# Kernel optimization log

Measured on AMD Instinct MI355X. Metric: run time of the kernel, lower is better.

Reference implementation:

```python
import jax, jax.numpy as jnp
import numpy as np

B, S, D, H = 2, 2048, 768, 12
DK = D // H
NEG = -1e9

def setup_inputs() -> dict:
    key = jax.random.key(0)
    ks = jax.random.split(key, 12)
    def lin(k):
        kw, kb = jax.random.split(k)
        lim = 1.0 / np.sqrt(D)
        W = jax.random.uniform(kw, (D, D), jnp.float32, -lim, lim)
        b = jax.random.uniform(kb, (D,), jnp.float32, -lim, lim)
        return W, b
    Wq, bq = lin(ks[0]); Wk, bk = lin(ks[1]); Wv, bv = lin(ks[2]); Wo, bo = lin(ks[3])
    query = jax.random.normal(ks[4], (B, S, D), jnp.float32)
    key_t = jax.random.normal(ks[5], (B, S, D), jnp.float32)
    value = jax.random.normal(ks[6], (B, S, D), jnp.float32)
    mask = jax.random.randint(ks[7], (B, S, S), 0, 2, jnp.int32)
    return {"query": query, "key": key_t, "value": value, "mask": mask,
            "Wq": Wq, "bq": bq, "Wk": Wk, "bk": bk, "Wv": Wv, "bv": bv,
            "Wo": Wo, "bo": bo}

def reference(query, key, value, mask, Wq, bq, Wk, bk, Wv, bv, Wo, bo):
    # project and split heads: [B,S,D] -> [B,H,S,DK]
    def proj(x, W, b):
        return (x @ W.T + b).reshape(B, S, H, DK).transpose(0, 2, 1, 3)
    q = proj(query, Wq, bq)
    k = proj(key, Wk, bk)
    v = proj(value, Wv, bv)
    scale = np.float32(1.0 / np.sqrt(DK))
    scores = jnp.einsum('bhqd,bhkd->bhqk', q, k) * scale  # [B,H,S,S]
    scores = jnp.where(mask[:, None, :, :] == 0, jnp.float32(NEG), scores)
    log_attn = jax.nn.log_softmax(scores, axis=-1)  # [B,H,S,S]
    p_attn = jnp.exp(log_attn)                      # softmax, shares reduction
    x = jnp.einsum('bhqk,bhkd->bhqd', p_attn, v)    # [B,H,S,DK]
    x = x.transpose(0, 2, 1, 3).reshape(B, S, D)
    out = x @ Wo.T + bo
    return out, log_attn
```

## Files before the change

kernel.cpp:

```cpp
#include <hip/hip_runtime.h>

#define B_ 2
#define S_ 2048
#define D_ 768
#define H_ 12
#define DK_ 64
#define BH_ (B_*H_)
#define NEGV (-1e9f)
#define SCALE 0.125f
#define MINIT (-1e30f)

typedef unsigned short u16;
typedef unsigned long long u64;
typedef __attribute__((ext_vector_type(8))) short bf16x8;
typedef __attribute__((ext_vector_type(4))) float f32x4;
typedef __attribute__((ext_vector_type(4))) int   i32x4;

__device__ __forceinline__ u16 f2bf(float f){
  union { float f; unsigned int i; } v; v.f = f;
  unsigned int x = v.i;
  return (u16)((x + 0x7FFFu + ((x >> 16) & 1u)) >> 16);
}
__device__ __forceinline__ void split2(float x, u16& h, u16& l){
  const unsigned int xi = __float_as_uint(x);
  h = (u16)(xi >> 16);
  const float lo = x - __uint_as_float(xi & 0xFFFF0000u);
  l = (u16)(__float_as_uint(lo) >> 16);
}

#define XN_ ((size_t)4096*768)
#define WN_ ((size_t)768*768)

__global__ __launch_bounds__(256) void prep(
    const float* __restrict__ Xq, const float* __restrict__ Xk, const float* __restrict__ Xv,
    const float* __restrict__ Wq, const float* __restrict__ Wk, const float* __restrict__ Wv,
    const int* __restrict__ mask,
    u16* __restrict__ scr, u64* __restrict__ mbits)
{
  const int a = blockIdx.y;
  if (a == 6){
    const size_t nw = (size_t)B_*S_*(S_/64);
    for (size_t wi = (size_t)blockIdx.x*256 + threadIdx.x; wi < nw; wi += (size_t)gridDim.x*256){
      const int* mp = mask + wi*64;
      u64 v = 0;
      #pragma unroll
      for (int j=0;j<64;j+=4){
        i32x4 m4 = __builtin_nontemporal_load((const i32x4*)(mp + j));
        v |= ((u64)(m4.x!=0) << j)     | ((u64)(m4.y!=0) << (j+1))
           | ((u64)(m4.z!=0) << (j+2)) | ((u64)(m4.w!=0) << (j+3));
      }
      mbits[wi] = v;
    }
    return;
  }
  const float* src; u16* h; u16* l; size_t n;
  if (a < 3){
    src = (a==0)?Xq:(a==1)?Xk:Xv;
    h = scr + (size_t)a*XN_;  l = scr + (size_t)(3+a)*XN_;  n = XN_;
  } else {
    const int z = a-3;
    src = (z==0)?Wq:(z==1)?Wk:Wv;
    h = scr + 6*XN_ + (size_t)z*WN_;  l = scr + 6*XN_ + 3*WN_ + (size_t)z*WN_;  n = WN_;
  }
  const size_t nv = n >> 2;
  for (size_t i = (size_t)blockIdx.x*256 + threadIdx.x; i < nv; i += (size_t)gridDim.x*256){
    f32x4 v = __builtin_nontemporal_load((const f32x4*)src + i);
    ushort4 hv, lv;
    split2(v.x,hv.x,lv.x); split2(v.y,hv.y,lv.y); split2(v.z,hv.z,lv.z); split2(v.w,hv.w,lv.w);
    ((ushort4*)h)[i] = hv;  ((ushort4*)l)[i] = lv;
  }
}

template<bool ALO, bool BPRE, int OMODE>
__device__ __forceinline__ void gemmM(const u16* __restrict__ Ah_, const u16* __restrict__ Al_,
                                      const u16* __restrict__ Bh_, const u16* __restrict__ Bl_,
                                      const float* __restrict__ Bf_,
                                      const float* __restrict__ bias, void* __restrict__ outp)
{
  const int bx = blockIdx.x, by = blockIdx.y;
  const int tid  = threadIdx.x;
  const int lane = tid & 63;
  const int w    = tid >> 6;
  const int g    = lane >> 4;
  const int c    = lane & 15;
  const int wr   = w >> 1, wc = w & 1;

  __shared__ u16 Ah[128][36];
  __shared__ u16 Al[128][36];
  __shared__ u16 Bh[128][36];
  __shared__ u16 Bl[128][36];

  const int ar0 = (OMODE==2 ? by : bx) * 128;
  const int br0 = (OMODE==2 ? bx : by) * 128;

  const int prow = tid >> 2;
  const int pcol = (tid & 3) * 8;
  const int frow = tid >> 3;
  const int fcol = (tid & 7) * 4;

  uint4 rAh0, rAh1, rAl0, rAl1, rBh0, rBh1, rBl0, rBl1;
  float4 rf0, rf1, rf2, rf3;

  f32x4 acc[4][4];
  #pragma unroll
  for (int m=0;m<4;m++)
    #pragma unroll
    for (int n=0;n<4;n++) acc[m][n] = (f32x4){0.f,0.f,0.f,0.f};

#define LD_TILE(k0) do{ \
    rAh0 = *(const uint4*)(Ah_ + (size_t)(ar0+prow)*D_ + (k0) + pcol); \
    rAh1 = *(const uint4*)(Ah_ + (size_t)(ar0+64+prow)*D_ + (k0) + pcol); \
    if constexpr (ALO){ \
      rAl0 = *(const uint4*)(Al_ + (size_t)(ar0+prow)*D_ + (k0) + pcol); \
      rAl1 = *(const uint4*)(Al_ + (size_t)(ar0+64+prow)*D_ + (k0) + pcol); } \
    if constexpr (BPRE){ \
      rBh0 = *(const uint4*)(Bh_ + (size_t)(br0+prow)*D_ + (k0) + pcol); \
      rBh1 = *(const uint4*)(Bh_ + (size_t)(br0+64+prow)*D_ + (k0) + pcol); \
      rBl0 = *(const uint4*)(Bl_ + (size_t)(br0+prow)*D_ + (k0) + pcol); \
      rBl1 = *(const uint4*)(Bl_ + (size_t)(br0+64+prow)*D_ + (k0) + pcol); \
    } else { \
      rf0 = *(const float4*)(Bf_ + (size_t)(br0+frow)*D_ + (k0) + fcol); \
      rf1 = *(const float4*)(Bf_ + (size_t)(br0+32+frow)*D_ + (k0) + fcol); \
      rf2 = *(const float4*)(Bf_ + (size_t)(br0+64+frow)*D_ + (k0) + fcol); \
      rf3 = *(const float4*)(Bf_ + (size_t)(br0+96+frow)*D_ + (k0) + fcol); \
    } }while(0)

#define ST_F32(rf, rofs) do{ \
    ushort4 hv, lv; \
    split2((rf).x,hv.x,lv.x); split2((rf).y,hv.y,lv.y); \
    split2((rf).z,hv.z,lv.z); split2((rf).w,hv.w,lv.w); \
    *(ushort4*)&Bh[(rofs)+frow][fcol] = hv;  *(ushort4*)&Bl[(rofs)+frow][fcol] = lv; }while(0)

#define ST_TILE() do{ \
    *(uint4*)&Ah[prow][pcol] = rAh0;  *(uint4*)&Ah[prow+64][pcol] = rAh1; \
    if constexpr (ALO){ *(uint4*)&Al[prow][pcol] = rAl0; *(uint4*)&Al[prow+64][pcol] = rAl1; } \
    if constexpr (BPRE){ \
      *(uint4*)&Bh[prow][pcol] = rBh0;  *(uint4*)&Bh[prow+64][pcol] = rBh1; \
      *(uint4*)&Bl[prow][pcol] = rBl0;  *(uint4*)&Bl[prow+64][pcol] = rBl1; \
    } else { ST_F32(rf0,0); ST_F32(rf1,32); ST_F32(rf2,64); ST_F32(rf3,96); } }while(0)

  LD_TILE(0);

  for (int t=0; t<D_/32; ++t){
    __syncthreads();
    ST_TILE();
    if (t < D_/32 - 1) LD_TILE((t+1)*32);
    __syncthreads();

    bf16x8 fah[4], fal[4], fbh[4], fbl[4];
    #pragma unroll
    for (int m=0;m<4;m++){
      fah[m] = *(const bf16x8*)&Ah[wr*64 + m*16 + c][g*8];
      if constexpr (ALO) fal[m] = *(const bf16x8*)&Al[wr*64 + m*16 + c][g*8];
    }
    #pragma unroll
    for (int n=0;n<4;n++){
      fbh[n] = *(const bf16x8*)&Bh[wc*64 + n*16 + c][g*8];
      fbl[n] = *(const bf16x8*)&Bl[wc*64 + n*16 + c][g*8];
    }
    #pragma unroll
    for (int m=0;m<4;m++)
      #pragma unroll
      for (int n=0;n<4;n++){
        acc[m][n] = __builtin_amdgcn_mfma_f32_16x16x32_bf16(fah[m], fbh[n], acc[m][n], 0,0,0);
        acc[m][n] = __builtin_amdgcn_mfma_f32_16x16x32_bf16(fah[m], fbl[n], acc[m][n], 0,0,0);
        if constexpr (ALO)
          acc[m][n] = __builtin_amdgcn_mfma_f32_16x16x32_bf16(fal[m], fbh[n], acc[m][n], 0,0,0);
      }
  }
#undef LD_TILE
#undef ST_F32
#undef ST_TILE

  if constexpr (OMODE==0) {
    float* out = (float*)outp;
    float bb[4];
    #pragma unroll
    for (int n=0;n<4;n++) bb[n] = bias[br0 + wc*64 + n*16 + c];
    #pragma unroll
    for (int m=0;m<4;m++)
      #pragma unroll
      for (int r=0;r<4;r++){
        const int rg = ar0 + wr*64 + m*16 + g*4 + r;
        #pragma unroll
        for (int n=0;n<4;n++)
          out[(size_t)rg*D_ + br0 + wc*64 + n*16 + c] = acc[m][n][r] + bb[n];
      }
  } else if constexpr (OMODE==1) {
    u16* out = (u16*)outp;
    float bb[4];
    #pragma unroll
    for (int n=0;n<4;n++) bb[n] = bias[br0 + wc*64 + n*16 + c];
    #pragma unroll
    for (int m=0;m<4;m++)
      #pragma unroll
      for (int r=0;r<4;r++){
        const int rg = ar0 + wr*64 + m*16 + g*4 + r;
        const int batch = rg >> 11, s = rg & (S_-1);
        #pragma unroll
        for (int n=0;n<4;n++){
          const int col = br0 + wc*64 + n*16 + c;
          const int hh = col >> 6, dk = col & 63;
          out[((size_t)(batch*H_ + hh)*S_ + s)*DK_ + dk] = f2bf(acc[m][n][r] + bb[n]);
        }
      }
  } else {
    u16* out = (u16*)outp;
    #pragma unroll
    for (int m=0;m<4;m++)
      #pragma unroll
      for (int r=0;r<4;r++){
        const int dkg = ar0 + wr*64 + m*16 + g*4 + r;
        const int hh = dkg >> 6, dkl = dkg & 63;
        const float bb = bias[dkg];
        #pragma unroll
        for (int n=0;n<4;n++){
          const int sg = br0 + wc*64 + n*16 + c;
          const int batch = sg >> 11, s = sg & (S_-1);
          out[((size_t)(batch*H_ + hh)*DK_ + dkl)*S_ + s] = f2bf(acc[m][n][r] + bb);
        }
      }
  }
}

__global__ __launch_bounds__(256,2) void proj_qkv(
    const u16* __restrict__ scr,
    const float* __restrict__ bq, const float* __restrict__ bk, const float* __restrict__ bv,
    u16* __restrict__ qkv)
{
  const int z = blockIdx.z;
  u16* out = qkv + (size_t)z * ((size_t)BH_*S_*DK_);
  const u16* Xh = scr + (size_t)z*XN_;
  const u16* Xl = scr + (size_t)(3+z)*XN_;
  const u16* Wh = scr + 6*XN_ + (size_t)z*WN_;
  const u16* Wl = scr + 6*XN_ + 3*WN_ + (size_t)z*WN_;
  const float* bias = (z==0)?bq:(z==1)?bk:bv;
  if (z==2) gemmM<true,true,2>(Wh, Wl, Xh, Xl, nullptr, bias, (void*)out);
  else      gemmM<true,true,1>(Xh, Xl, Wh, Wl, nullptr, bias, (void*)out);
}

__global__ __launch_bounds__(256,2) void proj_o(
    const u16* __restrict__ Xc, const float* __restrict__ Wo, const float* __restrict__ bo,
    float* __restrict__ out)
{
  gemmM<false,false,0>(Xc, nullptr, nullptr, nullptr, Wo, bo, (void*)out);
}

__global__ __launch_bounds__(256,3) void attn(const u16* __restrict__ qkv,
                                              const u64* __restrict__ mbits,
                                              float* __restrict__ la, u16* __restrict__ ctx)
{
  const int bh = blockIdx.y;
  const int q0 = blockIdx.x * 64;
  const int b = bh / H_;
  const int h = bh - b*H_;
  const u16* Qp = qkv + (size_t)bh * S_ * DK_;
  const u16* Kp = qkv + (size_t)(BH_ + bh) * S_ * DK_;
  const u16* Vt = qkv + (size_t)(2*BH_ + bh) * S_ * DK_;
  const u64* Mb = mbits + (size_t)b * S_ * (S_/64);

  const int tid  = threadIdx.x;
  const int w    = tid >> 6;
  const int lane = tid & 63;
  const int g    = lane >> 4;
  const int c    = lane & 15;
  const int srow = tid >> 3;
  const int scol = (tid & 7) * 8;

  __shared__ u16 KsB[2][64][72];
  __shared__ u16 VsB[2][64][72];
  __shared__ u16 Ps[4][16][72];

  {
    uint4 qa = *(const uint4*)(Qp + (size_t)(q0+srow)*DK_ + scol);
    uint4 qb = *(const uint4*)(Qp + (size_t)(q0+32+srow)*DK_ + scol);
    *(uint4*)&VsB[0][srow][scol] = qa;
    *(uint4*)&VsB[0][srow+32][scol] = qb;
  }
  __syncthreads();
  const bf16x8 qf0 = *(const bf16x8*)&VsB[0][w*16 + c][g*8];
  const bf16x8 qf1 = *(const bf16x8*)&VsB[0][w*16 + c][g*8 + 32];

  float mt[4], lt[4];
  #pragma unroll
  for (int r=0;r<4;r++){ mt[r] = MINIT; lt[r] = 0.f; }

  {
    uint4 ka = *(const uint4*)(Kp + (size_t)srow*DK_ + scol);
    uint4 kb = *(const uint4*)(Kp + (size_t)(32+srow)*DK_ + scol);
    *(uint4*)&KsB[0][srow][scol] = ka;
    *(uint4*)&KsB[0][srow+32][scol] = kb;
    for (int t=0; t<S_/64; ++t){
      __syncthreads();
      if (t < S_/64-1){
        const u16* kp = Kp + (size_t)(t+1)*64*DK_;
        ka = *(const uint4*)(kp + (size_t)srow*DK_ + scol);
        kb = *(const uint4*)(kp + (size_t)(32+srow)*DK_ + scol);
      }
      u64 mw[4];
      #pragma unroll
      for (int r=0;r<4;r++) mw[r] = Mb[(size_t)(q0 + w*16 + g*4 + r)*(S_/64) + t];

      f32x4 sc[4];
      __builtin_amdgcn_s_setprio(1);
      #pragma unroll
      for (int nt=0; nt<4; nt++){
        const bf16x8 kf0 = *(const bf16x8*)&KsB[t&1][nt*16 + c][g*8];
        const bf16x8 kf1 = *(const bf16x8*)&KsB[t&1][nt*16 + c][g*8 + 32];
        f32x4 z = {0.f,0.f,0.f,0.f};
        z      = __builtin_amdgcn_mfma_f32_16x16x32_bf16(qf0, kf0, z, 0,0,0);
        sc[nt] = __builtin_amdgcn_mfma_f32_16x16x32_bf16(qf1, kf1, z, 0,0,0);
      }
      __builtin_amdgcn_s_setprio(0);
      #pragma unroll
      for (int r=0;r<4;r++){
        const float sv0 = ((mw[r] >> (c    )) & 1) ? sc[0][r]*SCALE : NEGV;
        const float sv1 = ((mw[r] >> (c+16)) & 1) ? sc[1][r]*SCALE : NEGV;
        const float sv2 = ((mw[r] >> (c+32)) & 1) ? sc[2][r]*SCALE : NEGV;
        const float sv3 = ((mw[r] >> (c+48)) & 1) ? sc[3][r]*SCALE : NEGV;
        const float cm = fmaxf(fmaxf(sv0,sv1), fmaxf(sv2,sv3));
        if (!__all(cm <= mt[r])){
          const float mn = fmaxf(mt[r], cm);
          lt[r] *= __expf(mt[r]-mn);
          mt[r] = mn;
        }
        lt[r] += __expf(sv0-mt[r]) + __expf(sv1-mt[r]) + __expf(sv2-mt[r]) + __expf(sv3-mt[r]);
      }
      if (t < S_/64-1){
        *(uint4*)&KsB[(t+1)&1][srow][scol] = ka;
        *(uint4*)&KsB[(t+1)&1][srow+32][scol] = kb;
      }
    }
  }

  float ml[4];
  #pragma unroll
  for (int r=0;r<4;r++){
    float m = mt[r], l = lt[r];
    #pragma unroll
    for (int st=1; st<16; st<<=1){
      const float m2 = __shfl_xor(m, st);
      const float l2 = __shfl_xor(l, st);
      const float mn = fmaxf(m, m2);
      l = l*__expf(m-mn) + l2*__expf(m2-mn);
      m = mn;
    }
    ml[r] = m + __logf(fmaxf(l, 1e-30f));
  }

  f32x4 o[4];
  #pragma unroll
  for (int nt=0;nt<4;nt++) o[nt] = (f32x4){0.f,0.f,0.f,0.f};

  {
    uint4 ka = *(const uint4*)(Kp + (size_t)srow*DK_ + scol);
    uint4 kb = *(const uint4*)(Kp + (size_t)(32+srow)*DK_ + scol);
    uint4 va = *(const uint4*)(Vt + (size_t)srow*S_ + scol);
    uint4 vb = *(const uint4*)(Vt + (size_t)(32+srow)*S_ + scol);
    *(uint4*)&KsB[0][srow][scol] = ka;   *(uint4*)&KsB[0][srow+32][scol] = kb;
    *(uint4*)&VsB[0][srow][scol] = va;   *(uint4*)&VsB[0][srow+32][scol] = vb;
    for (int t=0; t<S_/64; ++t){
      __syncthreads();
      if (t < S_/64-1){
        const u16* kp = Kp + (size_t)(t+1)*64*DK_;
        const u16* vp = Vt + (size_t)(t+1)*64;
        ka = *(const uint4*)(kp + (size_t)srow*DK_ + scol);
        kb = *(const uint4*)(kp + (size_t)(32+srow)*DK_ + scol);
        va = *(const uint4*)(vp + (size_t)srow*S_ + scol);
        vb = *(const uint4*)(vp + (size_t)(32+srow)*S_ + scol);
      }
      u64 mw[4];
      #pragma unroll
      for (int r=0;r<4;r++) mw[r] = Mb[(size_t)(q0 + w*16 + g*4 + r)*(S_/64) + t];

      f32x4 sc[4];
      __builtin_amdgcn_s_setprio(1);
      #pragma unroll
      for (int nt=0; nt<4; nt++){
        const bf16x8 kf0 = *(const bf16x8*)&KsB[t&1][nt*16 + c][g*8];
        const bf16x8 kf1 = *(const bf16x8*)&KsB[t&1][nt*16 + c][g*8 + 32];
        f32x4 z = {0.f,0.f,0.f,0.f};
        z      = __builtin_amdgcn_mfma_f32_16x16x32_bf16(qf0, kf0, z, 0,0,0);
        sc[nt] = __builtin_amdgcn_mfma_f32_16x16x32_bf16(qf1, kf1, z, 0,0,0);
      }
      __builtin_amdgcn_s_setprio(0);
      #pragma unroll
      for (int r=0;r<4;r++){
        float* lrow = la + ((size_t)bh*S_ + q0 + w*16 + g*4 + r)*S_ + (size_t)t*64 + c;
        #pragma unroll
        for (int nt=0;nt<4;nt++){
          const float s  = ((mw[r] >> (nt*16 + c)) & 1) ? sc[nt][r]*SCALE : NEGV;
          const float lv = fminf(s - ml[r], 0.f);
          Ps[w][g*4+r][nt*16 + c] = f2bf(__expf(lv));
          __builtin_nontemporal_store(lv, lrow + nt*16);
        }
      }
      const bf16x8 pf0 = *(const bf16x8*)&Ps[w][c][g*8];
      const bf16x8 pf1 = *(const bf16x8*)&Ps[w][c][g*8 + 32];
      __builtin_amdgcn_s_setprio(1);
      #pragma unroll
      for (int nt=0; nt<4; nt++){
        const bf16x8 vf0 = *(const bf16x8*)&VsB[t&1][nt*16 + c][g*8];
        const bf16x8 vf1 = *(const bf16x8*)&VsB[t&1][nt*16 + c][g*8 + 32];
        o[nt] = __builtin_amdgcn_mfma_f32_16x16x32_bf16(pf0, vf0, o[nt], 0,0,0);
        o[nt] = __builtin_amdgcn_mfma_f32_16x16x32_bf16(pf1, vf1, o[nt], 0,0,0);
      }
      __builtin_amdgcn_s_setprio(0);
      if (t < S_/64-1){
        *(uint4*)&KsB[(t+1)&1][srow][scol] = ka;   *(uint4*)&KsB[(t+1)&1][srow+32][scol] = kb;
        *(uint4*)&VsB[(t+1)&1][srow][scol] = va;   *(uint4*)&VsB[(t+1)&1][srow+32][scol] = vb;
      }
    }
  }

  #pragma unroll
  for (int r=0;r<4;r++){
    const int qi = q0 + w*16 + g*4 + r;
    u16* crow = ctx + ((size_t)b*S_ + qi)*D_ + h*DK_ + c;
    #pragma unroll
    for (int nt=0;nt<4;nt++) crow[nt*16] = f2bf(o[nt][r]);
  }
}

extern "C" void kernel_launch(void* const* d_in, const int* in_sizes, int n_in,
                              void* d_out, int out_size, void* d_ws, size_t ws_size,
                              hipStream_t stream)
{
  const float* query = (const float*)d_in[0];
  const float* key   = (const float*)d_in[1];
  const float* value = (const float*)d_in[2];
  const int* mask    = (const int*)d_in[3];
  const float* Wq = (const float*)d_in[4];  const float* bq = (const float*)d_in[5];
  const float* Wk = (const float*)d_in[6];  const float* bk = (const float*)d_in[7];
  const float* Wv = (const float*)d_in[8];  const float* bv = (const float*)d_in[9];
  const float* Wo = (const float*)d_in[10]; const float* bo = (const float*)d_in[11];

  float* out = (float*)d_out;
  float* la  = out + (size_t)B_*S_*D_;
  u16* qkvws = (u16*)d_ws;
  u16* ctx = qkvws + (size_t)3*BH_*S_*DK_;
  u16* scr = (u16*)la;
  u64* mbits = (u64*)out;

  prep    <<<dim3(768,7,1),    dim3(256,1,1), 0, stream>>>(query,key,value,Wq,Wk,Wv,mask,scr,mbits);
  proj_qkv<<<dim3(32,6,3),     dim3(256,1,1), 0, stream>>>(scr, bq,bk,bv, qkvws);
  attn    <<<dim3(S_/64,BH_,1),dim3(256,1,1), 0, stream>>>(qkvws, mbits, la, ctx);
  proj_o  <<<dim3(32,6,1),     dim3(256,1,1), 0, stream>>>(ctx, Wo, bo, out);
}
```

Baseline: 653.3 us.

## Use direct-to-LDS loads in QKV GEMM, base-2 softmax, XCD-aware attention mapping

```diff
diff --git a/kernel.cpp b/kernel.cpp
--- a/kernel.cpp
+++ b/kernel.cpp
@@ -6,8 +6,9 @@
 #define H_ 12
 #define DK_ 64
 #define BH_ (B_*H_)
-#define NEGV (-1e9f)
-#define SCALE 0.125f
+#define SCALE2 0.1803368801111204f
+#define NEGV2 (-1.442695e9f)
+#define LN2F 0.6931471805599453f
 #define MINIT (-1e30f)
 
 typedef unsigned short u16;
@@ -15,6 +16,12 @@
 typedef __attribute__((ext_vector_type(8))) short bf16x8;
 typedef __attribute__((ext_vector_type(4))) float f32x4;
 typedef __attribute__((ext_vector_type(4))) int   i32x4;
+
+typedef const __attribute__((address_space(1))) unsigned int* gas_t;
+typedef __attribute__((address_space(3))) unsigned int* las_t;
+__device__ __forceinline__ void gload16(const u16* g, u16* l){
+  __builtin_amdgcn_global_load_lds((gas_t)g, (las_t)l, 16, 0, 0);
+}
 
 __device__ __forceinline__ u16 f2bf(float f){
   union { float f; unsigned int i; } v; v.f = f;
@@ -71,11 +78,10 @@
   }
 }
 
-template<bool ALO, bool BPRE, int OMODE>
-__device__ __forceinline__ void gemmM(const u16* __restrict__ Ah_, const u16* __restrict__ Al_,
+template<int OMODE>
+__device__ __forceinline__ void gemmG(const u16* __restrict__ Ah_, const u16* __restrict__ Al_,
                                       const u16* __restrict__ Bh_, const u16* __restrict__ Bl_,
-                                      const float* __restrict__ Bf_,
-                                      const float* __restrict__ bias, void* __restrict__ outp)
+                                      const float* __restrict__ bias, u16* __restrict__ out)
 {
   const int bx = blockIdx.x, by = blockIdx.y;
   const int tid  = threadIdx.x;
@@ -84,79 +90,49 @@
   const int g    = lane >> 4;
   const int c    = lane & 15;
   const int wr   = w >> 1, wc = w & 1;
-
-  __shared__ u16 Ah[128][36];
-  __shared__ u16 Al[128][36];
-  __shared__ u16 Bh[128][36];
-  __shared__ u16 Bl[128][36];
+  const int lrow = lane >> 2;
+  const int lcol = (lane & 3) * 8;
+
+  __shared__ u16 AhB[2][128][32];
+  __shared__ u16 AlB[2][128][32];
+  __shared__ u16 BhB[2][128][32];
+  __shared__ u16 BlB[2][128][32];
 
   const int ar0 = (OMODE==2 ? by : bx) * 128;
   const int br0 = (OMODE==2 ? bx : by) * 128;
 
-  const int prow = tid >> 2;
-  const int pcol = (tid & 3) * 8;
-  const int frow = tid >> 3;
-  const int fcol = (tid & 7) * 4;
-
-  uint4 rAh0, rAh1, rAl0, rAl1, rBh0, rBh1, rBl0, rBl1;
-  float4 rf0, rf1, rf2, rf3;
-
   f32x4 acc[4][4];
   #pragma unroll
   for (int m=0;m<4;m++)
     #pragma unroll
     for (int n=0;n<4;n++) acc[m][n] = (f32x4){0.f,0.f,0.f,0.f};
 
-#define LD_TILE(k0) do{ \
-    rAh0 = *(const uint4*)(Ah_ + (size_t)(ar0+prow)*D_ + (k0) + pcol); \
-    rAh1 = *(const uint4*)(Ah_ + (size_t)(ar0+64+prow)*D_ + (k0) + pcol); \
-    if constexpr (ALO){ \
-      rAl0 = *(const uint4*)(Al_ + (size_t)(ar0+prow)*D_ + (k0) + pcol); \
-      rAl1 = *(const uint4*)(Al_ + (size_t)(ar0+64+prow)*D_ + (k0) + pcol); } \
-    if constexpr (BPRE){ \
-      rBh0 = *(const uint4*)(Bh_ + (size_t)(br0+prow)*D_ + (k0) + pcol); \
-      rBh1 = *(const uint4*)(Bh_ + (size_t)(br0+64+prow)*D_ + (k0) + pcol); \
-      rBl0 = *(const uint4*)(Bl_ + (size_t)(br0+prow)*D_ + (k0) + pcol); \
-      rBl1 = *(const uint4*)(Bl_ + (size_t)(br0+64+prow)*D_ + (k0) + pcol); \
-    } else { \
-      rf0 = *(const float4*)(Bf_ + (size_t)(br0+frow)*D_ + (k0) + fcol); \
-      rf1 = *(const float4*)(Bf_ + (size_t)(br0+32+frow)*D_ + (k0) + fcol); \
-      rf2 = *(const float4*)(Bf_ + (size_t)(br0+64+frow)*D_ + (k0) + fcol); \
-      rf3 = *(const float4*)(Bf_ + (size_t)(br0+96+frow)*D_ + (k0) + fcol); \
+#define STAGE_G(b, k0) do{ \
+    _Pragma("unroll") \
+    for (int ch=0; ch<2; ch++){ \
+      const int rb = ch*64 + w*16; \
+      gload16(Ah_ + (size_t)(ar0+rb+lrow)*D_ + (k0) + lcol, &AhB[b][rb][0]); \
+      gload16(Al_ + (size_t)(ar0+rb+lrow)*D_ + (k0) + lcol, &AlB[b][rb][0]); \
+      gload16(Bh_ + (size_t)(br0+rb+lrow)*D_ + (k0) + lcol, &BhB[b][rb][0]); \
+      gload16(Bl_ + (size_t)(br0+rb+lrow)*D_ + (k0) + lcol, &BlB[b][rb][0]); \
     } }while(0)
 
-#define ST_F32(rf, rofs) do{ \
-    ushort4 hv, lv; \
-    split2((rf).x,hv.x,lv.x); split2((rf).y,hv.y,lv.y); \
-    split2((rf).z,hv.z,lv.z); split2((rf).w,hv.w,lv.w); \
-    *(ushort4*)&Bh[(rofs)+frow][fcol] = hv;  *(ushort4*)&Bl[(rofs)+frow][fcol] = lv; }while(0)
-
-#define ST_TILE() do{ \
-    *(uint4*)&Ah[prow][pcol] = rAh0;  *(uint4*)&Ah[prow+64][pcol] = rAh1; \
-    if constexpr (ALO){ *(uint4*)&Al[prow][pcol] = rAl0; *(uint4*)&Al[prow+64][pcol] = rAl1; } \
-    if constexpr (BPRE){ \
-      *(uint4*)&Bh[prow][pcol] = rBh0;  *(uint4*)&Bh[prow+64][pcol] = rBh1; \
-      *(uint4*)&Bl[prow][pcol] = rBl0;  *(uint4*)&Bl[prow+64][pcol] = rBl1; \
-    } else { ST_F32(rf0,0); ST_F32(rf1,32); ST_F32(rf2,64); ST_F32(rf3,96); } }while(0)
-
-  LD_TILE(0);
+  STAGE_G(0, 0);
 
   for (int t=0; t<D_/32; ++t){
     __syncthreads();
-    ST_TILE();
-    if (t < D_/32 - 1) LD_TILE((t+1)*32);
-    __syncthreads();
-
+    if (t < D_/32 - 1) STAGE_G((t+1)&1, (t+1)*32);
+    const int b = t&1;
     bf16x8 fah[4], fal[4], fbh[4], fbl[4];
     #pragma unroll
     for (int m=0;m<4;m++){
-      fah[m] = *(const bf16x8*)&Ah[wr*64 + m*16 + c][g*8];
-      if constexpr (ALO) fal[m] = *(const bf16x8*)&Al[wr*64 + m*16 + c][g*8];
+      fah[m] = *(const bf16x8*)&AhB[b][wr*64 + m*16 + c][g*8];
+      fal[m] = *(const bf16x8*)&AlB[b][wr*64 + m*16 + c][g*8];
     }
     #pragma unroll
     for (int n=0;n<4;n++){
-      fbh[n] = *(const bf16x8*)&Bh[wc*64 + n*16 + c][g*8];
-      fbl[n] = *(const bf16x8*)&Bl[wc*64 + n*16 + c][g*8];
+      fbh[n] = *(const bf16x8*)&BhB[b][wc*64 + n*16 + c][g*8];
+      fbl[n] = *(const bf16x8*)&BlB[b][wc*64 + n*16 + c][g*8];
     }
     #pragma unroll
     for (int m=0;m<4;m++)
@@ -164,30 +140,12 @@
       for (int n=0;n<4;n++){
         acc[m][n] = __builtin_amdgcn_mfma_f32_16x16x32_bf16(fah[m], fbh[n], acc[m][n], 0,0,0);
         acc[m][n] = __builtin_amdgcn_mfma_f32_16x16x32_bf16(fah[m], fbl[n], acc[m][n], 0,0,0);
-        if constexpr (ALO)
-          acc[m][n] = __builtin_amdgcn_mfma_f32_16x16x32_bf16(fal[m], fbh[n], acc[m][n], 0,0,0);
-      }
-  }
-#undef LD_TILE
-#undef ST_F32
-#undef ST_TILE
-
-  if constexpr (OMODE==0) {
-    float* out = (float*)outp;
-    float bb[4];
-    #pragma unroll
-    for (int n=0;n<4;n++) bb[n] = bias[br0 + wc*64 + n*16 + c];
-    #pragma unroll
-    for (int m=0;m<4;m++)
-      #pragma unroll
-      for (int r=0;r<4;r++){
-        const int rg = ar0 + wr*64 + m*16 + g*4 + r;
-        #pragma unroll
-        for (int n=0;n<4;n++)
-          out[(size_t)rg*D_ + br0 + wc*64 + n*16 + c] = acc[m][n][r] + bb[n];
-      }
-  } else if constexpr (OMODE==1) {
-    u16* out = (u16*)outp;
+        acc[m][n] = __builtin_amdgcn_mfma_f32_16x16x32_bf16(fal[m], fbh[n], acc[m][n], 0,0,0);
+      }
+  }
+#undef STAGE_G
+
+  if constexpr (OMODE==1) {
     float bb[4];
     #pragma unroll
     for (int n=0;n<4;n++) bb[n] = bias[br0 + wc*64 + n*16 + c];
@@ -205,7 +163,6 @@
         }
       }
   } else {
-    u16* out = (u16*)outp;
     #pragma unroll
     for (int m=0;m<4;m++)
       #pragma unroll
@@ -235,23 +192,112 @@
   const u16* Wh = scr + 6*XN_ + (size_t)z*WN_;
   const u16* Wl = scr + 6*XN_ + 3*WN_ + (size_t)z*WN_;
   const float* bias = (z==0)?bq:(z==1)?bk:bv;
-  if (z==2) gemmM<true,true,2>(Wh, Wl, Xh, Xl, nullptr, bias, (void*)out);
-  else      gemmM<true,true,1>(Xh, Xl, Wh, Wl, nullptr, bias, (void*)out);
+  if (z==2) gemmG<2>(Wh, Wl, Xh, Xl, bias, out);
+  else      gemmG<1>(Xh, Xl, Wh, Wl, bias, out);
 }
 
 __global__ __launch_bounds__(256,2) void proj_o(
     const u16* __restrict__ Xc, const float* __restrict__ Wo, const float* __restrict__ bo,
     float* __restrict__ out)
 {
-  gemmM<false,false,0>(Xc, nullptr, nullptr, nullptr, Wo, bo, (void*)out);
+  const int bx = blockIdx.x, by = blockIdx.y;
+  const int tid  = threadIdx.x;
+  const int lane = tid & 63;
+  const int w    = tid >> 6;
+  const int g    = lane >> 4;
+  const int c    = lane & 15;
+  const int wr   = w >> 1, wc = w & 1;
+
+  __shared__ u16 Ah[128][36];
+  __shared__ u16 Bh[128][36];
+  __shared__ u16 Bl[128][36];
+
+  const int ar0 = bx * 128;
+  const int br0 = by * 128;
+
+  const int prow = tid >> 2;
+  const int pcol = (tid & 3) * 8;
+  const int frow = tid >> 3;
+  const int fcol = (tid & 7) * 4;
+
+  uint4 rAh0, rAh1;
+  float4 rf0, rf1, rf2, rf3;
+
+  f32x4 acc[4][4];
+  #pragma unroll
+  for (int m=0;m<4;m++)
+    #pragma unroll
+    for (int n=0;n<4;n++) acc[m][n] = (f32x4){0.f,0.f,0.f,0.f};
+
+#define LD_TILE(k0) do{ \
+    rAh0 = *(const uint4*)(Xc + (size_t)(ar0+prow)*D_ + (k0) + pcol); \
+    rAh1 = *(const uint4*)(Xc + (size_t)(ar0+64+prow)*D_ + (k0) + pcol); \
+    rf0 = *(const float4*)(Wo + (size_t)(br0+frow)*D_ + (k0) + fcol); \
+    rf1 = *(const float4*)(Wo + (size_t)(br0+32+frow)*D_ + (k0) + fcol); \
+    rf2 = *(const float4*)(Wo + (size_t)(br0+64+frow)*D_ + (k0) + fcol); \
+    rf3 = *(const float4*)(Wo + (size_t)(br0+96+frow)*D_ + (k0) + fcol); }while(0)
+
+#define ST_F32(rf, rofs) do{ \
+    ushort4 hv, lv; \
+    split2((rf).x,hv.x,lv.x); split2((rf).y,hv.y,lv.y); \
+    split2((rf).z,hv.z,lv.z); split2((rf).w,hv.w,lv.w); \
+    *(ushort4*)&Bh[(rofs)+frow][fcol] = hv;  *(ushort4*)&Bl[(rofs)+frow][fcol] = lv; }while(0)
+
+#define ST_TILE() do{ \
+    *(uint4*)&Ah[prow][pcol] = rAh0;  *(uint4*)&Ah[prow+64][pcol] = rAh1; \
+    ST_F32(rf0,0); ST_F32(rf1,32); ST_F32(rf2,64); ST_F32(rf3,96); }while(0)
+
+  LD_TILE(0);
+
+  for (int t=0; t<D_/32; ++t){
+    __syncthreads();
+    ST_TILE();
+    if (t < D_/32 - 1) LD_TILE((t+1)*32);
+    __syncthreads();
+
+    bf16x8 fah[4], fbh[4], fbl[4];
+    #pragma unroll
+    for (int m=0;m<4;m++) fah[m] = *(const bf16x8*)&Ah[wr*64 + m*16 + c][g*8];
+    #pragma unroll
+    for (int n=0;n<4;n++){
+      fbh[n] = *(const bf16x8*)&Bh[wc*64 + n*16 + c][g*8];
+      fbl[n] = *(const bf16x8*)&Bl[wc*64 + n*16 + c][g*8];
+    }
+    #pragma unroll
+    for (int m=0;m<4;m++)
+      #pragma unroll
+      for (int n=0;n<4;n++){
+        acc[m][n] = __builtin_amdgcn_mfma_f32_16x16x32_bf16(fah[m], fbh[n], acc[m][n], 0,0,0);
+        acc[m][n] = __builtin_amdgcn_mfma_f32_16x16x32_bf16(fah[m], fbl[n], acc[m][n], 0,0,0);
+      }
+  }
+#undef LD_TILE
+#undef ST_F32
+#undef ST_TILE
+
+  float bb[4];
+  #pragma unroll
+  for (int n=0;n<4;n++) bb[n] = bo[br0 + wc*64 + n*16 + c];
+  #pragma unroll
+  for (int m=0;m<4;m++)
+    #pragma unroll
+    for (int r=0;r<4;r++){
+      const int rg = ar0 + wr*64 + m*16 + g*4 + r;
+      #pragma unroll
+      for (int n=0;n<4;n++)
+        out[(size_t)rg*D_ + br0 + wc*64 + n*16 + c] = acc[m][n][r] + bb[n];
+    }
 }
 
 __global__ __launch_bounds__(256,3) void attn(const u16* __restrict__ qkv,
                                               const u64* __restrict__ mbits,
                                               float* __restrict__ la, u16* __restrict__ ctx)
 {
-  const int bh = blockIdx.y;
-  const int q0 = blockIdx.x * 64;
+  const int n0   = blockIdx.x;
+  const int xcd  = n0 & 7;
+  const int mIdx = n0 >> 3;
+  const int bh   = xcd*3 + (mIdx >> 5);
+  const int q0   = (mIdx & 31) * 64;
   const int b = bh / H_;
   const int h = bh - b*H_;
   const u16* Qp = qkv + (size_t)bh * S_ * DK_;
@@ -314,17 +360,17 @@
       __builtin_amdgcn_s_setprio(0);
       #pragma unroll
       for (int r=0;r<4;r++){
-        const float sv0 = ((mw[r] >> (c    )) & 1) ? sc[0][r]*SCALE : NEGV;
-        const float sv1 = ((mw[r] >> (c+16)) & 1) ? sc[1][r]*SCALE : NEGV;
-        const float sv2 = ((mw[r] >> (c+32)) & 1) ? sc[2][r]*SCALE : NEGV;
-        const float sv3 = ((mw[r] >> (c+48)) & 1) ? sc[3][r]*SCALE : NEGV;
+        const float sv0 = ((mw[r] >> (c    )) & 1) ? sc[0][r]*SCALE2 : NEGV2;
+        const float sv1 = ((mw[r] >> (c+16)) & 1) ? sc[1][r]*SCALE2 : NEGV2;
+        const float sv2 = ((mw[r] >> (c+32)) & 1) ? sc[2][r]*SCALE2 : NEGV2;
+        const float sv3 = ((mw[r] >> (c+48)) & 1) ? sc[3][r]*SCALE2 : NEGV2;
         const float cm = fmaxf(fmaxf(sv0,sv1), fmaxf(sv2,sv3));
         if (!__all(cm <= mt[r])){
           const float mn = fmaxf(mt[r], cm);
-          lt[r] *= __expf(mt[r]-mn);
+          lt[r] *= exp2f(mt[r]-mn);
           mt[r] = mn;
         }
-        lt[r] += __expf(sv0-mt[r]) + __expf(sv1-mt[r]) + __expf(sv2-mt[r]) + __expf(sv3-mt[r]);
+        lt[r] += exp2f(sv0-mt[r]) + exp2f(sv1-mt[r]) + exp2f(sv2-mt[r]) + exp2f(sv3-mt[r]);
       }
       if (t < S_/64-1){
         *(uint4*)&KsB[(t+1)&1][srow][scol] = ka;
@@ -342,10 +388,10 @@
       const float m2 = __shfl_xor(m, st);
       const float l2 = __shfl_xor(l, st);
       const float mn = fmaxf(m, m2);
-      l = l*__expf(m-mn) + l2*__expf(m2-mn);
+      l = l*exp2f(m-mn) + l2*exp2f(m2-mn);
       m = mn;
     }
-    ml[r] = m + __logf(fmaxf(l, 1e-30f));
+    ml[r] = m + __log2f(fmaxf(l, 1e-30f));
   }
 
   f32x4 o[4];
@@ -389,10 +435,10 @@
         float* lrow = la + ((size_t)bh*S_ + q0 + w*16 + g*4 + r)*S_ + (size_t)t*64 + c;
         #pragma unroll
         for (int nt=0;nt<4;nt++){
-          const float s  = ((mw[r] >> (nt*16 + c)) & 1) ? sc[nt][r]*SCALE : NEGV;
-          const float lv = fminf(s - ml[r], 0.f);
-          Ps[w][g*4+r][nt*16 + c] = f2bf(__expf(lv));
-          __builtin_nontemporal_store(lv, lrow + nt*16);
+          const float s2 = ((mw[r] >> (nt*16 + c)) & 1) ? sc[nt][r]*SCALE2 : NEGV2;
+          const float d2 = fminf(s2 - ml[r], 0.f);
+          Ps[w][g*4+r][nt*16 + c] = f2bf(exp2f(d2));
+          __builtin_nontemporal_store(d2 * LN2F, lrow + nt*16);
         }
       }
       const bf16x8 pf0 = *(const bf16x8*)&Ps[w][c][g*8];
@@ -442,8 +488,8 @@
   u16* scr = (u16*)la;
   u64* mbits = (u64*)out;
 
-  prep    <<<dim3(768,7,1),    dim3(256,1,1), 0, stream>>>(query,key,value,Wq,Wk,Wv,mask,scr,mbits);
-  proj_qkv<<<dim3(32,6,3),     dim3(256,1,1), 0, stream>>>(scr, bq,bk,bv, qkvws);
-  attn    <<<dim3(S_/64,BH_,1),dim3(256,1,1), 0, stream>>>(qkvws, mbits, la, ctx);
-  proj_o  <<<dim3(32,6,1),     dim3(256,1,1), 0, stream>>>(ctx, Wo, bo, out);
-}
+  prep    <<<dim3(768,7,1),   dim3(256,1,1), 0, stream>>>(query,key,value,Wq,Wk,Wv,mask,scr,mbits);
+  proj_qkv<<<dim3(32,6,3),    dim3(256,1,1), 0, stream>>>(scr, bq,bk,bv, qkvws);
+  attn    <<<dim3(768,1,1),   dim3(256,1,1), 0, stream>>>(qkvws, mbits, la, ctx);
+  proj_o  <<<dim3(32,6,1),    dim3(256,1,1), 0, stream>>>(ctx, Wo, bo, out);
+}
```

Result: slower. 710.2 us (+8.7%).
